# Optimization experiments

Hardware: AMD Instinct MI355X
Metric: run time of the kernel (lower is better)

## Reference

```python
import jax, jax.numpy as jnp
import numpy as np

R_MAX = 5.0
AVG_NEIGH = 16.0
F = 64          # hidden scalar channels (hidden_irreps count of 0e)
NB = 8          # num_bessel
LMAX = 2
S = 9           # (LMAX+1)^2 spherical-harmonic components
NE = 10         # num_elements
G = 4           # num_graphs
T = 2           # num_interactions
L_OF_LM = np.array([0, 1, 1, 1, 2, 2, 2, 2, 2])


def spherical_harmonics(u):
    # real SH up to l=2, e3nn 'component' normalization; u: [E,3] unit vectors
    x, y, z = u[:, 0], u[:, 1], u[:, 2]
    s3, s5, s15 = 3.0 ** 0.5, 5.0 ** 0.5, 15.0 ** 0.5
    return jnp.stack([
        jnp.ones_like(x),
        s3 * x, s3 * y, s3 * z,
        s15 * x * y, s15 * y * z, (s5 / 2.0) * (3.0 * z * z - 1.0),
        s15 * x * z, (s15 / 2.0) * (x * x - y * y),
    ], axis=-1)  # [E, 9]


def radial_embedding(r):
    # Bessel basis * polynomial cutoff (p=5), as in MACE RadialEmbeddingBlock
    r_safe = jnp.maximum(r, 1e-6)
    n = jnp.arange(1, NB + 1, dtype=r.dtype)  # [NB]
    bessel = jnp.sqrt(2.0 / R_MAX) * jnp.sin(n[None, :] * jnp.pi * r_safe[:, None] / R_MAX) / r_safe[:, None]
    u = r / R_MAX
    p = 5.0
    f = (1.0 - 0.5 * (p + 1) * (p + 2) * u ** 5 + p * (p + 2) * u ** 6 - 0.5 * p * (p + 1) * u ** 7)
    f = f * (u < 1.0)
    return bessel * f[:, None]  # [E, NB]


def setup_inputs() -> dict:
    key = jax.random.key(0)
    ks = jax.random.split(key, 24)
    N, E = 20000, 320000
    positions = jax.random.normal(ks[0], (N, 3), dtype=jnp.float32) * 5.0
    species = jax.random.randint(ks[1], (N,), 0, NE)
    node_attrs = jax.nn.one_hot(species, NE, dtype=jnp.float32)
    edge_index = jax.random.randint(ks[2], (2, E), 0, N)
    shifts = jnp.zeros((E, 3), dtype=jnp.float32)
    batch = jnp.sort(jax.random.randint(ks[3], (N,), 0, G)).astype(jnp.int32)
    charges = jax.random.normal(ks[4], (N,), dtype=jnp.float32) * 0.1
    sc = 1.0 / np.sqrt(F)
    params = {
        'atomic_energies': jax.random.normal(ks[5], (NE,), dtype=jnp.float32),
        'W_embed': jax.random.normal(ks[6], (NE, F), dtype=jnp.float32),
        'Wr0': jax.random.normal(ks[7], (T, NB, 64), dtype=jnp.float32) / np.sqrt(NB),
        'Wr1': jax.random.normal(ks[8], (T, 64, 64), dtype=jnp.float32) / 8.0,
        'Wr2': jax.random.normal(ks[9], (T, 64, F * (LMAX + 1)), dtype=jnp.float32) / 8.0,
        'Wmix': jax.random.normal(ks[10], (T, LMAX + 1, F, F), dtype=jnp.float32) * sc,
        'Wprod': jax.random.normal(ks[11], (T, NE, F, 3), dtype=jnp.float32) * sc,
        'Wread0': jax.random.normal(ks[12], (F,), dtype=jnp.float32) * sc,
        'Wm1': jax.random.normal(ks[13], (F, 16), dtype=jnp.float32) * sc,
        'wm2': jax.random.normal(ks[14], (16,), dtype=jnp.float32) * 0.25,
        'Wq': jax.random.normal(ks[15], (T, F), dtype=jnp.float32) * sc,
    }
    return dict(positions=positions, node_attrs=node_attrs, shifts=shifts,
                charges=charges, edge_index=edge_index, batch=batch, **params)


def _forward(positions, node_attrs, shifts, charges,
             atomic_energies, W_embed, Wr0, Wr1, Wr2, Wmix, Wprod,
             Wread0, Wm1, wm2, Wq, edge_index, batch):
    N = positions.shape[0]
    src, dst = edge_index[0], edge_index[1]
    # isolated-atom reference energies
    node_e0 = node_attrs @ atomic_energies                       # [N]
    e0 = jax.ops.segment_sum(node_e0, batch, num_segments=G)     # [G]
    # edge geometry
    vec = positions[dst] - positions[src] + shifts               # [E,3]
    lengths = jnp.linalg.norm(vec, axis=-1)                      # [E]
    len_safe = jnp.where(lengths > 1e-6, lengths, 1.0)
    unit = vec / len_safe[:, None]
    edge_attrs = spherical_harmonics(unit)                       # [E,S]
    edge_feats = radial_embedding(lengths)                       # [E,NB]
    # node embedding: scalars only, rest of irreps zero
    node_feats = jnp.zeros((N, F, S), dtype=positions.dtype)
    node_feats = node_feats.at[:, :, 0].set(node_attrs @ W_embed)
    charge_density = charges[:, None] * jnp.ones((1, 1), positions.dtype)  # [N,1] formal charges (l=0)
    lm = jnp.asarray(L_OF_LM)
    energy = e0
    for t in range(T):
        # radial MLP -> per-edge tensor-product weights [E,F,LMAX+1]
        h = jax.nn.silu(edge_feats @ Wr0[t])
        h = jax.nn.silu(h @ Wr1[t])
        w = (h @ Wr2[t]).reshape(-1, F, LMAX + 1)
        wl = w[:, :, lm]                                         # [E,F,S]
        s_src = node_feats[src, :, 0]                            # [E,F] gather
        msg = wl * s_src[:, :, None] * edge_attrs[:, None, :]    # [E,F,S]
        A = jax.ops.segment_sum(msg, dst, num_segments=N) / AVG_NEIGH  # [N,F,S] scatter
        # per-l linear channel mixing
        A = jnp.einsum('nfs,sfg->ngs', A, Wmix[t][lm])
        # symmetric product basis (correlation 3), element-dependent weights
        wp = jnp.einsum('ne,efc->nfc', node_attrs, Wprod[t])     # [N,F,3]
        p1 = A[:, :, 0]                                          # scalar invariant
        p2 = jnp.sum(A * A, axis=-1)                             # norm invariant
        scale = wp[:, :, 0] + wp[:, :, 1] * p1 + wp[:, :, 2] * p2
        new_feats = A * scale[:, :, None]
        if t > 0:
            new_feats = new_feats + node_feats                   # residual self-connection
        node_feats = new_feats
        scal = node_feats[:, :, 0]
        if t == T - 1:
            node_en = jax.nn.silu(scal @ Wm1) @ wm2              # nonlinear readout
        else:
            node_en = scal @ Wread0                              # linear readout
        energy = energy + jax.ops.segment_sum(node_en, batch, num_segments=G)
        charge_density = charge_density + (scal @ Wq[t])[:, None]
    return energy  # [G]


def reference(positions, node_attrs, shifts, charges, edge_index, batch,
              atomic_energies, W_embed, Wr0, Wr1, Wr2, Wmix, Wprod,
              Wread0, Wm1, wm2, Wq):
    return _forward(positions, node_attrs, shifts, charges,
                    atomic_energies, W_embed, Wr0, Wr1, Wr2, Wmix, Wprod,
                    Wread0, Wm1, wm2, Wq, edge_index, batch)
```

## Files before the change

### kernel.cpp

```cpp
#include <hip/hip_runtime.h>
#include <hip/hip_bf16.h>

#define F 64
#define NB 8
#define NE 10
#define GSEG 4
#define EPW 256
#define NTAB 2048

__device__ __forceinline__ float silu(float x) {
    return x / (1.0f + __expf(-x));
}

__device__ __forceinline__ float bcast(float v, int lane) {
    return __uint_as_float(__builtin_amdgcn_readlane(__float_as_uint(v), lane));
}

__global__ __launch_bounds__(256) void init_and_tables(
    const float* __restrict__ node_attrs, const float* __restrict__ AE,
    const float* __restrict__ W_embed, const int* __restrict__ batch,
    const float* __restrict__ pos,
    float* __restrict__ S0, float* __restrict__ epart,
    int* __restrict__ deg, float4* __restrict__ pos4, int N, int nodeBlocks,
    const float* __restrict__ Wr0, const float* __restrict__ Wr1,
    const float* __restrict__ Wr2, float* __restrict__ Tab)
{
    int w = threadIdx.x >> 6, lane = threadIdx.x & 63;

    if (blockIdx.x < (unsigned)nodeBlocks) {
        int n = blockIdx.x * 4 + w;
        if (n >= N) return;
        float sc = 0.0f, e0 = 0.0f;
        #pragma unroll
        for (int e = 0; e < NE; e++) {
            float a = node_attrs[n * NE + e];
            sc = fmaf(a, W_embed[e * F + lane], sc);
            e0 = fmaf(a, AE[e], e0);
        }
        S0[(size_t)n * F + lane] = sc;
        if (lane == 0) {
            deg[n] = 0;
            pos4[n] = make_float4(pos[n * 3], pos[n * 3 + 1], pos[n * 3 + 2], 0.f);
            atomicAdd(&epart[batch[n] * EPW + (n & (EPW - 1))], e0);
        }
        return;
    }

    const int blocksPerTab = (NTAB + 1 + 3) / 4;
    int bid = blockIdx.x - nodeBlocks;
    int tab = bid / blocksPerTab;
    int eidx = (bid - tab * blocksPerTab) * 4 + w;
    if (eidx > NTAB) return;
    const float* W0 = Wr0 + tab * 512;
    const float* W1 = Wr1 + tab * 4096;
    const float* W2 = Wr2 + tab * 12288;

    float r = (float)eidx * (5.0f / NTAB);
    float rs = fmaxf(r, 1e-6f);
    float s1, c1;
    __sincosf(0.6283185307179586f * rs, &s1, &c1);
    float u = r * 0.2f;
    float u2 = u * u, u4 = u2 * u2, u5 = u4 * u, u6 = u5 * u, u7 = u6 * u;
    float fc = 1.0f - 21.0f * u5 + 35.0f * u6 - 15.0f * u7;
    float pref = 0.6324555320336759f / rs * fc;
    float ef[NB];
    {
        float sp = 0.0f, sc_ = s1, tc = 2.0f * c1;
        #pragma unroll
        for (int k = 0; k < NB; k++) {
            ef[k] = pref * sc_;
            float sn = tc * sc_ - sp;
            sp = sc_; sc_ = sn;
        }
    }

    float a1 = 0.0f;
    #pragma unroll
    for (int k = 0; k < NB; k++) a1 = fmaf(ef[k], W0[k * 64 + lane], a1);
    float h1 = silu(a1);

    float a2 = 0.0f;
    #pragma unroll 8
    for (int k = 0; k < 64; k++)
        a2 = fmaf(bcast(h1, k), W1[k * 64 + lane], a2);
    float h2 = silu(a2);

    float w0 = 0.f, w1 = 0.f, w2 = 0.f;
    #pragma unroll 8
    for (int k = 0; k < 64; k++) {
        float hk = bcast(h2, k);
        const float* wr = W2 + k * 192 + lane * 3;
        w0 = fmaf(hk, wr[0], w0);
        w1 = fmaf(hk, wr[1], w1);
        w2 = fmaf(hk, wr[2], w2);
    }

    float* Trow = Tab + ((size_t)tab * (NTAB + 1) + eidx) * 192;
    Trow[lane] = w0;
    Trow[64 + lane] = w1;
    Trow[128 + lane] = w2;
}

__global__ __launch_bounds__(256) void edge_prep(
    const float4* __restrict__ pos4, const float* __restrict__ shifts,
    const int* __restrict__ EI, int E,
    float4* __restrict__ geoFull, int* __restrict__ deg)
{
    int e = blockIdx.x * 256 + threadIdx.x;
    if (e >= E) return;
    int s = EI[e], d = EI[E + e];
    float4 pd = pos4[d], ps = pos4[s];
    float vx = pd.x - ps.x + shifts[e * 3 + 0];
    float vy = pd.y - ps.y + shifts[e * 3 + 1];
    float vz = pd.z - ps.z + shifts[e * 3 + 2];
    float len = sqrtf(vx * vx + vy * vy + vz * vz);
    float ls = (len > 1e-6f) ? len : 1.0f;
    float inv = 1.0f / ls;
    geoFull[e] = make_float4(vx * inv, vy * inv, vz * inv, len);
    if (len < 5.0f) atomicAdd(&deg[d], 1);
}

__global__ __launch_bounds__(256) void alloc_start(
    const int* __restrict__ deg, int* __restrict__ start,
    int* __restrict__ cursor, int* __restrict__ total, int N)
{
    __shared__ int wsum[4];
    __shared__ int gbase;
    int t = threadIdx.x;
    int n = blockIdx.x * 256 + t;
    int lane = t & 63, w = t >> 6;
    int v = (n < N) ? deg[n] : 0;
    int inc = v;
    #pragma unroll
    for (int off = 1; off < 64; off <<= 1) {
        int u = __shfl_up(inc, off);
        if (lane >= off) inc += u;
    }
    if (lane == 63) wsum[w] = inc;
    __syncthreads();
    if (t == 0) {
        int s0 = wsum[0], s1 = wsum[1], s2 = wsum[2], s3 = wsum[3];
        int bs = s0 + s1 + s2 + s3;
        wsum[0] = 0; wsum[1] = s0; wsum[2] = s0 + s1; wsum[3] = s0 + s1 + s2;
        gbase = atomicAdd(total, bs);
    }
    __syncthreads();
    if (n < N) {
        int st = gbase + wsum[w] + (inc - v);
        start[n] = st;
        cursor[n] = st;
    }
}

__global__ __launch_bounds__(256) void csr_fill(
    const float4* __restrict__ geoFull, const int* __restrict__ EI, int E,
    int* __restrict__ cursor,
    float4* __restrict__ geoS, int* __restrict__ srcS, int EB)
{
    int e = blockIdx.x * 256 + threadIdx.x;
    if (e >= E) return;
    float4 gv = geoFull[e];
    if (gv.w < 5.0f) {
        int d = EI[E + e];
        int p = atomicAdd(&cursor[d], 1);
        if (p < EB) {
            geoS[p] = gv;
            srcS[p] = EI[e];
        }
    }
}

template <int PHASE>
__global__ __launch_bounds__(256) void gather_node(
    const float4* __restrict__ geoS, const int* __restrict__ srcS,
    const float* __restrict__ Tab,
    const int* __restrict__ start, const int* __restrict__ deg,
    const float* __restrict__ Wmixt, const float* __restrict__ Wprodt,
    const float* __restrict__ node_attrs, const int* __restrict__ batch,
    const float* __restrict__ Wread0, const float* __restrict__ Wm1,
    const float* __restrict__ wm2,
    const float* __restrict__ Sin, float* __restrict__ Sout,
    float* __restrict__ epart, int N)
{
    __shared__ float As[4][768];

    int g = threadIdx.x & 63;
    int w = threadIdx.x >> 6;
    int n = blockIdx.x * 4 + w;
    if (n >= N) return;

    int st = start[n], dg = deg[n];
    int b = batch[n];

    if (dg == 0) {
        if (PHASE == 0) {
            Sout[(size_t)n * F + g] = 0.0f;
        } else {
            float sc0 = Sin[(size_t)n * F + g];
            int gi = g & 15;
            float acc = 0.0f;
            #pragma unroll 8
            for (int k = 0; k < 64; k++)
                acc = fmaf(bcast(sc0, k), Wm1[k * 16 + gi], acc);
            float v = (g < 16) ? silu(acc) * wm2[gi] : 0.0f;
            #pragma unroll
            for (int off = 32; off > 0; off >>= 1) v += __shfl_xor(v, off);
            if (g == 0) atomicAdd(&epart[b * EPW + (n & (EPW - 1))], v);
        }
        return;
    }

    float am0 = 0.f, am1 = 0.f, am2_ = 0.f, am3 = 0.f, am4 = 0.f,
          am5 = 0.f, am6 = 0.f, am7 = 0.f, am8 = 0.f;

    const float s3 = 1.7320508075688772f;
    const float s5h = 1.1180339887498948f;
    const float s15 = 3.8729833462074170f;
    const float s15h = 1.9364916731037085f;

    for (int i = st; i < st + dg; i++) {
        float4 gv = geoS[i];
        int srcn = srcS[i];
        float sv = Sin[(size_t)srcn * F + g];
        float scaled = gv.w * (NTAB / 5.0f);
        int idx = (int)scaled;
        float fr = scaled - (float)idx;
        const float* T0 = Tab + (size_t)idx * 192;
        float wa = T0[g],        wb = T0[192 + g];
        float wc = T0[64 + g],   wd = T0[256 + g];
        float we = T0[128 + g],  wf_ = T0[320 + g];
        float w0 = fmaf(fr, wb - wa, wa);
        float w1 = fmaf(fr, wd - wc, wc);
        float w2 = fmaf(fr, wf_ - we, we);

        float ux = gv.x, uy = gv.y, uz = gv.z;
        float m0 = w0 * sv, m1 = w1 * sv, m2 = w2 * sv;
        am0 += m0;
        am1 = fmaf(m1, s3 * ux, am1);
        am2_ = fmaf(m1, s3 * uy, am2_);
        am3 = fmaf(m1, s3 * uz, am3);
        am4 = fmaf(m2, s15 * ux * uy, am4);
        am5 = fmaf(m2, s15 * uy * uz, am5);
        am6 = fmaf(m2, s5h * (3.0f * uz * uz - 1.0f), am6);
        am7 = fmaf(m2, s15 * ux * uz, am7);
        am8 = fmaf(m2, s15h * (ux * ux - uy * uy), am8);
    }

    const float inv16 = 0.0625f;
    float* aw = As[w];
    *(float4*)&aw[g * 12]     = make_float4(am0 * inv16, am1 * inv16,
                                            am2_ * inv16, am3 * inv16);
    *(float4*)&aw[g * 12 + 4] = make_float4(am4 * inv16, am5 * inv16,
                                            am6 * inv16, am7 * inv16);
    aw[g * 12 + 8] = am8 * inv16;

    float b0 = 0.f, b1 = 0.f, b2 = 0.f, b3 = 0.f, b4 = 0.f,
          b5 = 0.f, b6 = 0.f, b7 = 0.f, b8 = 0.f;
    #pragma unroll 8
    for (int f = 0; f < 64; f++) {
        float w0 = Wmixt[f * 64 + g];
        float w1 = Wmixt[4096 + f * 64 + g];
        float w2 = Wmixt[8192 + f * 64 + g];
        float4 aA = *(const float4*)&aw[f * 12];
        float4 aB = *(const float4*)&aw[f * 12 + 4];
        float a8 = aw[f * 12 + 8];
        b0 = fmaf(aA.x, w0, b0);
        b1 = fmaf(aA.y, w1, b1);
        b2 = fmaf(aA.z, w1, b2);
        b3 = fmaf(aA.w, w1, b3);
        b4 = fmaf(aB.x, w2, b4);
        b5 = fmaf(aB.y, w2, b5);
        b6 = fmaf(aB.z, w2, b6);
        b7 = fmaf(aB.w, w2, b7);
        b8 = fmaf(a8, w2, b8);
    }

    float wp0 = 0.f, wp1 = 0.f, wp2 = 0.f;
    #pragma unroll
    for (int e = 0; e < NE; e++) {
        float a = node_attrs[n * NE + e];
        const float* W = Wprodt + (e * F + g) * 3;
        wp0 = fmaf(a, W[0], wp0);
        wp1 = fmaf(a, W[1], wp1);
        wp2 = fmaf(a, W[2], wp2);
    }
    float p1 = b0;
    float p2 = b0 * b0 + b1 * b1 + b2 * b2 + b3 * b3 + b4 * b4 +
               b5 * b5 + b6 * b6 + b7 * b7 + b8 * b8;
    float scale = wp0 + wp1 * p1 + wp2 * p2;
    float sc0 = b0 * scale;

    if (PHASE == 0) {
        Sout[(size_t)n * F + g] = sc0;
        float v = sc0 * Wread0[g];
        #pragma unroll
        for (int off = 32; off > 0; off >>= 1) v += __shfl_xor(v, off);
        if (g == 0) atomicAdd(&epart[b * EPW + (n & (EPW - 1))], v);
    } else {
        sc0 += Sin[(size_t)n * F + g];
        int gi = g & 15;
        float acc = 0.0f;
        #pragma unroll 8
        for (int k = 0; k < 64; k++)
            acc = fmaf(bcast(sc0, k), Wm1[k * 16 + gi], acc);
        float v = (g < 16) ? silu(acc) * wm2[gi] : 0.0f;
        #pragma unroll
        for (int off = 32; off > 0; off >>= 1) v += __shfl_xor(v, off);
        if (g == 0) atomicAdd(&epart[b * EPW + (n & (EPW - 1))], v);
    }
}

__global__ __launch_bounds__(256) void reduce_energy(
    const float* __restrict__ epart, float* __restrict__ out)
{
    int t = threadIdx.x;
    __shared__ float ps[GSEG][4];
    for (int b = 0; b < GSEG; b++) {
        float v = epart[b * EPW + t];
        #pragma unroll
        for (int off = 32; off > 0; off >>= 1) v += __shfl_xor(v, off);
        if ((t & 63) == 0) ps[b][t >> 6] = v;
    }
    __syncthreads();
    if (t < GSEG) out[t] = ps[t][0] + ps[t][1] + ps[t][2] + ps[t][3];
}

extern "C" void kernel_launch(void* const* d_in, const int* in_sizes, int n_in,
                              void* d_out, int out_size, void* d_ws, size_t ws_size,
                              hipStream_t stream) {
    const float* positions  = (const float*)d_in[0];
    const float* node_attrs = (const float*)d_in[1];
    const float* shifts     = (const float*)d_in[2];
    const int*   edge_index = (const int*)d_in[4];
    const int*   batch      = (const int*)d_in[5];
    const float* AE         = (const float*)d_in[6];
    const float* W_embed    = (const float*)d_in[7];
    const float* Wr0        = (const float*)d_in[8];
    const float* Wr1        = (const float*)d_in[9];
    const float* Wr2        = (const float*)d_in[10];
    const float* Wmix       = (const float*)d_in[11];
    const float* Wprod      = (const float*)d_in[12];
    const float* Wread0     = (const float*)d_in[13];
    const float* Wm1        = (const float*)d_in[14];
    const float* wm2        = (const float*)d_in[15];

    int N = in_sizes[0] / 3;
    int E = in_sizes[4] / 2;
    int EB = E / 8;
    float* out = (float*)d_out;

    char* ws = (char*)d_ws;
    size_t off = 0;
    float4* geoFull = (float4*)(ws + off); off += (size_t)E * sizeof(float4);
    float4* geoS  = (float4*)(ws + off); off += (size_t)EB * sizeof(float4);
    float4* pos4  = (float4*)(ws + off); off += (size_t)N * sizeof(float4);
    float*  S0    = (float*)(ws + off);  off += (size_t)N * F * sizeof(float);
    float*  S1    = (float*)(ws + off);  off += (size_t)N * F * sizeof(float);
    int*    srcS  = (int*)(ws + off);    off += (size_t)EB * sizeof(int);
    int*    deg   = (int*)(ws + off);    off += (size_t)N * sizeof(int);
    int*    start = (int*)(ws + off);    off += (size_t)N * sizeof(int);
    int*    cursor= (int*)(ws + off);    off += (size_t)N * sizeof(int);
    float*  epart = (float*)(ws + off);  off += GSEG * EPW * sizeof(float);
    int*    total = (int*)(ws + off);    off += 128;
    float*  Tab   = (float*)(ws + off);
    off += (size_t)2 * (NTAB + 1) * 192 * sizeof(float);

    hipMemsetAsync(epart, 0, GSEG * EPW * sizeof(float) + 128, stream);

    int nodeBlocks4 = (N + 3) / 4;
    int nodeBlocks256 = (N + 255) / 256;
    int edgeBlocks = (E + 255) / 256;
    int tabBlocks = 2 * ((NTAB + 1 + 3) / 4);
    int gatherBlocks = (N + 3) / 4;
    size_t tabStride = (size_t)(NTAB + 1) * 192;

    init_and_tables<<<nodeBlocks4 + tabBlocks, 256, 0, stream>>>(
        node_attrs, AE, W_embed, batch, positions,
        S0, epart, deg, pos4, N, nodeBlocks4,
        Wr0, Wr1, Wr2, Tab);
    edge_prep<<<edgeBlocks, 256, 0, stream>>>(pos4, shifts, edge_index, E,
                                              geoFull, deg);
    alloc_start<<<nodeBlocks256, 256, 0, stream>>>(deg, start, cursor, total, N);
    csr_fill<<<edgeBlocks, 256, 0, stream>>>(geoFull, edge_index, E,
                                             cursor, geoS, srcS, EB);

    gather_node<0><<<gatherBlocks, 256, 0, stream>>>(geoS, srcS, Tab, start, deg,
                                         Wmix, Wprod, node_attrs, batch,
                                         Wread0, Wm1, wm2, S0, S1, epart, N);
    gather_node<1><<<gatherBlocks, 256, 0, stream>>>(geoS, srcS, Tab + tabStride,
                                         start, deg,
                                         Wmix + 12288, Wprod + NE * F * 3,
                                         node_attrs, batch,
                                         Wread0, Wm1, wm2, S1, S1, epart, N);

    reduce_energy<<<1, 256, 0, stream>>>(epart, out);
}
```

Measured before the change: 222.4 us.

## Split gather and channel mixing, run mixing as bf16 MFMA over 16-node tiles

```diff
diff --git a/kernel.cpp b/kernel.cpp
--- a/kernel.cpp
+++ b/kernel.cpp
@@ -8,12 +8,21 @@
 #define EPW 256
 #define NTAB 2048
 
+typedef __attribute__((ext_vector_type(8))) short short8v;
+typedef __attribute__((ext_vector_type(4))) float float4v;
+
 __device__ __forceinline__ float silu(float x) {
     return x / (1.0f + __expf(-x));
 }
 
 __device__ __forceinline__ float bcast(float v, int lane) {
     return __uint_as_float(__builtin_amdgcn_readlane(__float_as_uint(v), lane));
+}
+
+__device__ __forceinline__ unsigned short f2bf(float x) {
+    unsigned int u = __float_as_uint(x);
+    u += 0x7FFFu + ((u >> 16) & 1u);
+    return (unsigned short)(u >> 16);
 }
 
 __global__ __launch_bounds__(256) void init_and_tables(
@@ -23,7 +32,9 @@
     float* __restrict__ S0, float* __restrict__ epart,
     int* __restrict__ deg, float4* __restrict__ pos4, int N, int nodeBlocks,
     const float* __restrict__ Wr0, const float* __restrict__ Wr1,
-    const float* __restrict__ Wr2, float* __restrict__ Tab)
+    const float* __restrict__ Wr2, float* __restrict__ Tab,
+    const float* __restrict__ Wmix, unsigned short* __restrict__ Wbt,
+    int tabBlocks)
 {
     int w = threadIdx.x >> 6, lane = threadIdx.x & 63;
 
@@ -43,6 +54,16 @@
             pos4[n] = make_float4(pos[n * 3], pos[n * 3 + 1], pos[n * 3 + 2], 0.f);
             atomicAdd(&epart[batch[n] * EPW + (n & (EPW - 1))], e0);
         }
+        return;
+    }
+
+    if (blockIdx.x >= (unsigned)(nodeBlocks + tabBlocks)) {
+        int i = (blockIdx.x - nodeBlocks - tabBlocks) * 256 + threadIdx.x;
+        if (i >= 2 * 3 * 4096) return;
+        int tl = i >> 12;
+        int gf = i & 4095;
+        int g = gf >> 6, f = gf & 63;
+        Wbt[i] = f2bf(Wmix[(size_t)(tl * 64 + f) * 64 + g] * 0.0625f);
         return;
     }
 
@@ -170,43 +191,23 @@
     }
 }
 
-template <int PHASE>
-__global__ __launch_bounds__(256) void gather_node(
+__global__ __launch_bounds__(256) void gather_edges(
     const float4* __restrict__ geoS, const int* __restrict__ srcS,
     const float* __restrict__ Tab,
     const int* __restrict__ start, const int* __restrict__ deg,
-    const float* __restrict__ Wmixt, const float* __restrict__ Wprodt,
-    const float* __restrict__ node_attrs, const int* __restrict__ batch,
-    const float* __restrict__ Wread0, const float* __restrict__ Wm1,
-    const float* __restrict__ wm2,
-    const float* __restrict__ Sin, float* __restrict__ Sout,
-    float* __restrict__ epart, int N)
-{
-    __shared__ float As[4][768];
-
+    const float* __restrict__ Sin, unsigned short* __restrict__ Abuf,
+    int N, int N16)
+{
     int g = threadIdx.x & 63;
     int w = threadIdx.x >> 6;
     int n = blockIdx.x * 4 + w;
     if (n >= N) return;
+    size_t PL = (size_t)N16 * 64;
 
     int st = start[n], dg = deg[n];
-    int b = batch[n];
-
     if (dg == 0) {
-        if (PHASE == 0) {
-            Sout[(size_t)n * F + g] = 0.0f;
-        } else {
-            float sc0 = Sin[(size_t)n * F + g];
-            int gi = g & 15;
-            float acc = 0.0f;
-            #pragma unroll 8
-            for (int k = 0; k < 64; k++)
-                acc = fmaf(bcast(sc0, k), Wm1[k * 16 + gi], acc);
-            float v = (g < 16) ? silu(acc) * wm2[gi] : 0.0f;
-            #pragma unroll
-            for (int off = 32; off > 0; off >>= 1) v += __shfl_xor(v, off);
-            if (g == 0) atomicAdd(&epart[b * EPW + (n & (EPW - 1))], v);
-        }
+        #pragma unroll
+        for (int s = 0; s < 9; s++) Abuf[s * PL + (size_t)n * 64 + g] = 0;
         return;
     }
 
@@ -246,67 +247,99 @@
         am8 = fmaf(m2, s15h * (ux * ux - uy * uy), am8);
     }
 
-    const float inv16 = 0.0625f;
-    float* aw = As[w];
-    *(float4*)&aw[g * 12]     = make_float4(am0 * inv16, am1 * inv16,
-                                            am2_ * inv16, am3 * inv16);
-    *(float4*)&aw[g * 12 + 4] = make_float4(am4 * inv16, am5 * inv16,
-                                            am6 * inv16, am7 * inv16);
-    aw[g * 12 + 8] = am8 * inv16;
-
-    float b0 = 0.f, b1 = 0.f, b2 = 0.f, b3 = 0.f, b4 = 0.f,
-          b5 = 0.f, b6 = 0.f, b7 = 0.f, b8 = 0.f;
-    #pragma unroll 8
-    for (int f = 0; f < 64; f++) {
-        float w0 = Wmixt[f * 64 + g];
-        float w1 = Wmixt[4096 + f * 64 + g];
-        float w2 = Wmixt[8192 + f * 64 + g];
-        float4 aA = *(const float4*)&aw[f * 12];
-        float4 aB = *(const float4*)&aw[f * 12 + 4];
-        float a8 = aw[f * 12 + 8];
-        b0 = fmaf(aA.x, w0, b0);
-        b1 = fmaf(aA.y, w1, b1);
-        b2 = fmaf(aA.z, w1, b2);
-        b3 = fmaf(aA.w, w1, b3);
-        b4 = fmaf(aB.x, w2, b4);
-        b5 = fmaf(aB.y, w2, b5);
-        b6 = fmaf(aB.z, w2, b6);
-        b7 = fmaf(aB.w, w2, b7);
-        b8 = fmaf(a8, w2, b8);
-    }
-
-    float wp0 = 0.f, wp1 = 0.f, wp2 = 0.f;
-    #pragma unroll
-    for (int e = 0; e < NE; e++) {
-        float a = node_attrs[n * NE + e];
-        const float* W = Wprodt + (e * F + g) * 3;
-        wp0 = fmaf(a, W[0], wp0);
-        wp1 = fmaf(a, W[1], wp1);
-        wp2 = fmaf(a, W[2], wp2);
-    }
-    float p1 = b0;
-    float p2 = b0 * b0 + b1 * b1 + b2 * b2 + b3 * b3 + b4 * b4 +
-               b5 * b5 + b6 * b6 + b7 * b7 + b8 * b8;
-    float scale = wp0 + wp1 * p1 + wp2 * p2;
-    float sc0 = b0 * scale;
-
-    if (PHASE == 0) {
-        Sout[(size_t)n * F + g] = sc0;
-        float v = sc0 * Wread0[g];
-        #pragma unroll
-        for (int off = 32; off > 0; off >>= 1) v += __shfl_xor(v, off);
-        if (g == 0) atomicAdd(&epart[b * EPW + (n & (EPW - 1))], v);
-    } else {
-        sc0 += Sin[(size_t)n * F + g];
-        int gi = g & 15;
-        float acc = 0.0f;
-        #pragma unroll 8
-        for (int k = 0; k < 64; k++)
-            acc = fmaf(bcast(sc0, k), Wm1[k * 16 + gi], acc);
-        float v = (g < 16) ? silu(acc) * wm2[gi] : 0.0f;
-        #pragma unroll
-        for (int off = 32; off > 0; off >>= 1) v += __shfl_xor(v, off);
-        if (g == 0) atomicAdd(&epart[b * EPW + (n & (EPW - 1))], v);
+    size_t base = (size_t)n * 64 + g;
+    Abuf[0 * PL + base] = f2bf(am0);
+    Abuf[1 * PL + base] = f2bf(am1);
+    Abuf[2 * PL + base] = f2bf(am2_);
+    Abuf[3 * PL + base] = f2bf(am3);
+    Abuf[4 * PL + base] = f2bf(am4);
+    Abuf[5 * PL + base] = f2bf(am5);
+    Abuf[6 * PL + base] = f2bf(am6);
+    Abuf[7 * PL + base] = f2bf(am7);
+    Abuf[8 * PL + base] = f2bf(am8);
+}
+
+template <int PHASE>
+__global__ __launch_bounds__(256) void mix_finish(
+    const unsigned short* __restrict__ Abuf,
+    const unsigned short* __restrict__ Wbt,
+    const float* __restrict__ Wprodt,
+    const float* __restrict__ node_attrs, const int* __restrict__ batch,
+    const float* __restrict__ Wread0, const float* __restrict__ Wm1,
+    const float* __restrict__ wm2,
+    const float* __restrict__ Sin, float* __restrict__ Sout,
+    float* __restrict__ epart, int N, int N16)
+{
+    __shared__ float Osh[9 * 1072];
+
+    int t = threadIdx.x;
+    int lane = t & 63, w = t >> 6;
+    int l15 = lane & 15, quad = lane >> 4;
+    int n0 = blockIdx.x * 16;
+    size_t PL = (size_t)N16 * 64;
+
+    for (int s = w; s < 9; s += 4) {
+        int l = (s == 0) ? 0 : ((s < 4) ? 1 : 2);
+        const unsigned short* Ap = Abuf + s * PL + (size_t)(n0 + l15) * 64;
+        const unsigned short* Bp = Wbt + l * 4096 + (size_t)l15 * 64;
+        short8v a0 = *(const short8v*)(Ap + quad * 8);
+        short8v a1 = *(const short8v*)(Ap + 32 + quad * 8);
+        #pragma unroll
+        for (int nt = 0; nt < 4; nt++) {
+            short8v b0 = *(const short8v*)(Bp + nt * 1024 + quad * 8);
+            short8v b1 = *(const short8v*)(Bp + nt * 1024 + 32 + quad * 8);
+            float4v acc = {0.f, 0.f, 0.f, 0.f};
+            acc = __builtin_amdgcn_mfma_f32_16x16x32_bf16(a0, b0, acc, 0, 0, 0);
+            acc = __builtin_amdgcn_mfma_f32_16x16x32_bf16(a1, b1, acc, 0, 0, 0);
+            #pragma unroll
+            for (int r = 0; r < 4; r++)
+                Osh[s * 1072 + (quad * 4 + r) * 67 + nt * 16 + l15] = acc[r];
+        }
+    }
+    __syncthreads();
+
+    for (int v = w; v < 16; v += 4) {
+        int n = n0 + v;
+        if (n >= N) continue;
+        int b = batch[n];
+        float bb[9];
+        #pragma unroll
+        for (int s = 0; s < 9; s++) bb[s] = Osh[s * 1072 + v * 67 + lane];
+
+        float wp0 = 0.f, wp1 = 0.f, wp2 = 0.f;
+        #pragma unroll
+        for (int e = 0; e < NE; e++) {
+            float a = node_attrs[n * NE + e];
+            const float* W = Wprodt + (e * F + lane) * 3;
+            wp0 = fmaf(a, W[0], wp0);
+            wp1 = fmaf(a, W[1], wp1);
+            wp2 = fmaf(a, W[2], wp2);
+        }
+        float p1 = bb[0];
+        float p2 = 0.f;
+        #pragma unroll
+        for (int s = 0; s < 9; s++) p2 = fmaf(bb[s], bb[s], p2);
+        float scale = wp0 + wp1 * p1 + wp2 * p2;
+        float sc0 = bb[0] * scale;
+
+        if (PHASE == 0) {
+            Sout[(size_t)n * F + lane] = sc0;
+            float vv = sc0 * Wread0[lane];
+            #pragma unroll
+            for (int off = 32; off > 0; off >>= 1) vv += __shfl_xor(vv, off);
+            if (lane == 0) atomicAdd(&epart[b * EPW + (n & (EPW - 1))], vv);
+        } else {
+            sc0 += Sin[(size_t)n * F + lane];
+            int gi = lane & 15;
+            float acc = 0.0f;
+            #pragma unroll 8
+            for (int k = 0; k < 64; k++)
+                acc = fmaf(bcast(sc0, k), Wm1[k * 16 + gi], acc);
+            float vv = (lane < 16) ? silu(acc) * wm2[gi] : 0.0f;
+            #pragma unroll
+            for (int off = 32; off > 0; off >>= 1) vv += __shfl_xor(vv, off);
+            if (lane == 0) atomicAdd(&epart[b * EPW + (n & (EPW - 1))], vv);
+        }
     }
 }
 
@@ -347,23 +380,30 @@
     int N = in_sizes[0] / 3;
     int E = in_sizes[4] / 2;
     int EB = E / 8;
+    int N16 = (N + 15) & ~15;
     float* out = (float*)d_out;
 
     char* ws = (char*)d_ws;
     size_t off = 0;
-    float4* geoFull = (float4*)(ws + off); off += (size_t)E * sizeof(float4);
-    float4* geoS  = (float4*)(ws + off); off += (size_t)EB * sizeof(float4);
-    float4* pos4  = (float4*)(ws + off); off += (size_t)N * sizeof(float4);
-    float*  S0    = (float*)(ws + off);  off += (size_t)N * F * sizeof(float);
-    float*  S1    = (float*)(ws + off);  off += (size_t)N * F * sizeof(float);
-    int*    srcS  = (int*)(ws + off);    off += (size_t)EB * sizeof(int);
-    int*    deg   = (int*)(ws + off);    off += (size_t)N * sizeof(int);
-    int*    start = (int*)(ws + off);    off += (size_t)N * sizeof(int);
-    int*    cursor= (int*)(ws + off);    off += (size_t)N * sizeof(int);
-    float*  epart = (float*)(ws + off);  off += GSEG * EPW * sizeof(float);
-    int*    total = (int*)(ws + off);    off += 128;
+    auto alignup = [](size_t v) { return (v + 255) & ~(size_t)255; };
+    float4* geoFull = (float4*)(ws + off); off = alignup(off + (size_t)E * sizeof(float4));
+    float4* geoS  = (float4*)(ws + off); off = alignup(off + (size_t)EB * sizeof(float4));
+    float4* pos4  = (float4*)(ws + off); off = alignup(off + (size_t)N * sizeof(float4));
+    float*  S0    = (float*)(ws + off);  off = alignup(off + (size_t)N * F * sizeof(float));
+    float*  S1    = (float*)(ws + off);  off = alignup(off + (size_t)N * F * sizeof(float));
+    int*    srcS  = (int*)(ws + off);    off = alignup(off + (size_t)EB * sizeof(int));
+    int*    deg   = (int*)(ws + off);    off = alignup(off + (size_t)N * sizeof(int));
+    int*    start = (int*)(ws + off);    off = alignup(off + (size_t)N * sizeof(int));
+    int*    cursor= (int*)(ws + off);    off = alignup(off + (size_t)N * sizeof(int));
+    float*  epart = (float*)(ws + off);
+    int*    total = (int*)(ws + off + GSEG * EPW * sizeof(float));
+    off = alignup(off + GSEG * EPW * sizeof(float) + 128);
     float*  Tab   = (float*)(ws + off);
-    off += (size_t)2 * (NTAB + 1) * 192 * sizeof(float);
+    off = alignup(off + (size_t)2 * (NTAB + 1) * 192 * sizeof(float));
+    unsigned short* Wbt = (unsigned short*)(ws + off);
+    off = alignup(off + (size_t)2 * 3 * 4096 * sizeof(unsigned short));
+    unsigned short* Abuf = (unsigned short*)(ws + off);
+    off += (size_t)9 * N16 * 64 * sizeof(unsigned short);
 
     hipMemsetAsync(epart, 0, GSEG * EPW * sizeof(float) + 128, stream);
 
@@ -371,27 +411,33 @@
     int nodeBlocks256 = (N + 255) / 256;
     int edgeBlocks = (E + 255) / 256;
     int tabBlocks = 2 * ((NTAB + 1 + 3) / 4);
-    int gatherBlocks = (N + 3) / 4;
+    int wbBlocks = (2 * 3 * 4096 + 255) / 256;
+    int mfBlocks = (N + 15) / 16;
     size_t tabStride = (size_t)(NTAB + 1) * 192;
 
-    init_and_tables<<<nodeBlocks4 + tabBlocks, 256, 0, stream>>>(
+    init_and_tables<<<nodeBlocks4 + tabBlocks + wbBlocks, 256, 0, stream>>>(
         node_attrs, AE, W_embed, batch, positions,
         S0, epart, deg, pos4, N, nodeBlocks4,
-        Wr0, Wr1, Wr2, Tab);
+        Wr0, Wr1, Wr2, Tab, Wmix, Wbt, tabBlocks);
     edge_prep<<<edgeBlocks, 256, 0, stream>>>(pos4, shifts, edge_index, E,
                                               geoFull, deg);
     alloc_start<<<nodeBlocks256, 256, 0, stream>>>(deg, start, cursor, total, N);
     csr_fill<<<edgeBlocks, 256, 0, stream>>>(geoFull, edge_index, E,
                                              cursor, geoS, srcS, EB);
 
-    gather_node<0><<<gatherBlocks, 256, 0, stream>>>(geoS, srcS, Tab, start, deg,
-                                         Wmix, Wprod, node_attrs, batch,
-                                         Wread0, Wm1, wm2, S0, S1, epart, N);
-    gather_node<1><<<gatherBlocks, 256, 0, stream>>>(geoS, srcS, Tab + tabStride,
-                                         start, deg,
-                                         Wmix + 12288, Wprod + NE * F * 3,
-                                         node_attrs, batch,
-                                         Wread0, Wm1, wm2, S1, S1, epart, N);
+    gather_edges<<<nodeBlocks4, 256, 0, stream>>>(geoS, srcS, Tab, start, deg,
+                                                  S0, Abuf, N, N16);
+    mix_finish<0><<<mfBlocks, 256, 0, stream>>>(Abuf, Wbt, Wprod,
+                                                node_attrs, batch,
+                                                Wread0, Wm1, wm2,
+                                                S0, S1, epart, N, N16);
+    gather_edges<<<nodeBlocks4, 256, 0, stream>>>(geoS, srcS, Tab + tabStride,
+                                                  start, deg, S1, Abuf, N, N16);
+    mix_finish<1><<<mfBlocks, 256, 0, stream>>>(Abuf, Wbt + 3 * 4096,
+                                                Wprod + NE * F * 3,
+                                                node_attrs, batch,
+                                                Wread0, Wm1, wm2,
+                                                S1, S1, epart, N, N16);
 
     reduce_energy<<<1, 256, 0, stream>>>(epart, out);
 }
```

New measurement: 242.5 us. 1.09x slower.
